# Performance work log

Measured on AMD Instinct MI355X. Metric: run time of the kernel, lower is better.

The kernel has to match this reference:

```python
import jax, jax.numpy as jnp
import numpy as np

UNITS = 256
D_IN = 256


def setup_inputs() -> dict:
    key = jax.random.key(0)
    ks = jax.random.split(key, 12)
    B, T, M, d, u = 16, 128, 512, D_IN, UNITS
    s = lambda fan_in: 1.0 / np.sqrt(fan_in)
    return {
        "inputs": jax.random.normal(ks[0], (B, T, d), jnp.float32),
        "attended_inputs": jax.random.normal(ks[1], (B, M, d), jnp.float32),
        # key_dense: Dense(units) applied to attended_inputs
        "key_W": jax.random.normal(ks[2], (d, u), jnp.float32) * s(d),
        "key_b": jnp.zeros((u,), jnp.float32),
        # query_dense: Dense(units) applied to state_h
        "query_W": jax.random.normal(ks[3], (u, u), jnp.float32) * s(u),
        "query_b": jnp.zeros((u,), jnp.float32),
        # attention_dense: Dense(1)
        "attn_W": jax.random.normal(ks[4], (u, 1), jnp.float32) * s(u),
        "attn_b": jnp.zeros((1,), jnp.float32),
        # LSTMCell built with input dim 2*d (inputs concat context); gate order i,f,g,o
        "lstm_W": jax.random.normal(ks[5], (2 * d, 4 * u), jnp.float32) * s(2 * d),
        "lstm_U": jax.random.normal(ks[6], (u, 4 * u), jnp.float32) * s(u),
        "lstm_b": jnp.zeros((4 * u,), jnp.float32),
    }


def reference(inputs, attended_inputs, key_W, key_b, query_W, query_b,
              attn_W, attn_b, lstm_W, lstm_U, lstm_b):
    B, T, d = inputs.shape
    u = lstm_U.shape[0]
    # keys computed once, shared across all timesteps: [B, M, u]
    keys = jnp.einsum('bmd,du->bmu', attended_inputs, key_W) + key_b
    aw = attn_W[:, 0]  # [u]

    def step(carry, x_t):
        h, c = carry                                   # [B,u], [B,u]
        q = h @ query_W + query_b                      # [B,u]
        e = jnp.tanh(keys + q[:, None, :])             # [B,M,u]
        scores = jnp.einsum('bmu,u->bm', e, aw) + attn_b[0]
        a = jax.nn.softmax(scores, axis=-1)            # [B,M]
        ctx = jnp.einsum('bm,bmd->bd', a, attended_inputs)
        xin = jnp.concatenate([x_t, ctx], axis=-1)     # [B,2d]
        z = xin @ lstm_W + h @ lstm_U + lstm_b         # [B,4u]
        i_g, f_g, g_g, o_g = jnp.split(z, 4, axis=-1)
        i_g = jax.nn.sigmoid(i_g)
        f_g = jax.nn.sigmoid(f_g)
        g_g = jnp.tanh(g_g)
        o_g = jax.nn.sigmoid(o_g)
        c_new = f_g * c + i_g * g_g
        h_new = o_g * jnp.tanh(c_new)
        return (h_new, c_new), h_new

    h0 = jnp.zeros((B, u), inputs.dtype)
    c0 = jnp.zeros((B, u), inputs.dtype)
    (hT, cT), ys = jax.lax.scan(step, (h0, c0), jnp.swapaxes(inputs, 0, 1))
    seq = jnp.swapaxes(ys, 0, 1)  # [B,T,u] (return_sequences=True)
    return seq, hT, cT
```

## Files before the change

kernel.cpp:

```cpp
#include <hip/hip_runtime.h>
#include <hip/hip_bf16.h>
#include <cstddef>

#define BATCH 16
#define TSTEPS 128
#define MSLOTS 512
#define DIN 256
#define UNITS 256
#define ZDIM 1024
#define G 8
#define NBLK (BATCH*G)
#define NTHR 1024

static __device__ __forceinline__ float tanhf_fast(float x) {
    float e = __expf(2.0f * x);
    return 1.0f - 2.0f / (e + 1.0f);
}
static __device__ __forceinline__ float sigmoidf_fast(float x) {
    return 1.0f / (1.0f + __expf(-x));
}
static __device__ __forceinline__ void st_agent_u(unsigned* p, unsigned v) {
    __hip_atomic_store(p, v, __ATOMIC_RELAXED, __HIP_MEMORY_SCOPE_AGENT);
}
static __device__ __forceinline__ unsigned ld_agent_u(const unsigned* p) {
    return __hip_atomic_load(p, __ATOMIC_RELAXED, __HIP_MEMORY_SCOPE_AGENT);
}
static __device__ __forceinline__ unsigned pack_bf(float a, float b) {
    unsigned ua = __float_as_uint(a); ua = (ua + 0x7fffu + ((ua >> 16) & 1u)) >> 16;
    unsigned ub = __float_as_uint(b); ub = ((ub + 0x7fffu + ((ub >> 16) & 1u)) >> 16) << 16;
    return ua | ub;
}
static __device__ __forceinline__ float bf_lo(unsigned w) { return __uint_as_float(w << 16); }
static __device__ __forceinline__ float bf_hi(unsigned w) { return __uint_as_float(w & 0xffff0000u); }

__global__ __launch_bounds__(256) void gemm_bias_kernel(
    const float* __restrict__ A, const float* __restrict__ B,
    const float* __restrict__ bias, float* __restrict__ C,
    int M, int N, int K)
{
    __shared__ float As[16][68];
    __shared__ float Bs[16][68];
    const int tid = threadIdx.x;
    const int bm = blockIdx.x * 64;
    const int bn = blockIdx.y * 64;
    const int tx = tid & 15, ty = tid >> 4;
    const int ar = tid >> 2, ac = (tid & 3) * 4;
    const int br = tid >> 4, bc = (tid & 15) * 4;
    float acc[4][4] = {};

    for (int k0 = 0; k0 < K; k0 += 16) {
        float4 av = *(const float4*)(A + (size_t)(bm + ar) * K + k0 + ac);
        float4 bv = *(const float4*)(B + (size_t)(k0 + br) * N + bn + bc);
        As[ac + 0][ar] = av.x; As[ac + 1][ar] = av.y;
        As[ac + 2][ar] = av.z; As[ac + 3][ar] = av.w;
        *(float4*)(&Bs[br][bc]) = bv;
        __syncthreads();
#pragma unroll
        for (int kk = 0; kk < 16; ++kk) {
            float a0 = As[kk][ty*4+0], a1 = As[kk][ty*4+1];
            float a2 = As[kk][ty*4+2], a3 = As[kk][ty*4+3];
            float b0 = Bs[kk][tx*4+0], b1 = Bs[kk][tx*4+1];
            float b2 = Bs[kk][tx*4+2], b3 = Bs[kk][tx*4+3];
            acc[0][0]+=a0*b0; acc[0][1]+=a0*b1; acc[0][2]+=a0*b2; acc[0][3]+=a0*b3;
            acc[1][0]+=a1*b0; acc[1][1]+=a1*b1; acc[1][2]+=a1*b2; acc[1][3]+=a1*b3;
            acc[2][0]+=a2*b0; acc[2][1]+=a2*b1; acc[2][2]+=a2*b2; acc[2][3]+=a2*b3;
            acc[3][0]+=a3*b0; acc[3][1]+=a3*b1; acc[3][2]+=a3*b2; acc[3][3]+=a3*b3;
        }
        __syncthreads();
    }
#pragma unroll
    for (int i = 0; i < 4; ++i)
#pragma unroll
        for (int j = 0; j < 4; ++j) {
            int cn = bn + tx * 4 + j;
            C[(size_t)(bm + ty * 4 + i) * N + cn] = acc[i][j] + bias[cn];
        }
}

__global__ __launch_bounds__(256) void gemm_T_bf16_kernel(
    const float* __restrict__ A, const float* __restrict__ B,
    unsigned short* __restrict__ CT, int M, int N, int K)
{
    __shared__ float As[16][68];
    __shared__ float Bs[16][68];
    __shared__ float Ts[64][65];
    const int tid = threadIdx.x;
    const int bm = blockIdx.x * 64;
    const int bn = blockIdx.y * 64;
    const int tx = tid & 15, ty = tid >> 4;
    const int ar = tid >> 2, ac = (tid & 3) * 4;
    const int br = tid >> 4, bc = (tid & 15) * 4;
    float acc[4][4] = {};

    for (int k0 = 0; k0 < K; k0 += 16) {
        float4 av = *(const float4*)(A + (size_t)(bm + ar) * K + k0 + ac);
        float4 bv = *(const float4*)(B + (size_t)(k0 + br) * N + bn + bc);
        As[ac + 0][ar] = av.x; As[ac + 1][ar] = av.y;
        As[ac + 2][ar] = av.z; As[ac + 3][ar] = av.w;
        *(float4*)(&Bs[br][bc]) = bv;
        __syncthreads();
#pragma unroll
        for (int kk = 0; kk < 16; ++kk) {
            float a0 = As[kk][ty*4+0], a1 = As[kk][ty*4+1];
            float a2 = As[kk][ty*4+2], a3 = As[kk][ty*4+3];
            float b0 = Bs[kk][tx*4+0], b1 = Bs[kk][tx*4+1];
            float b2 = Bs[kk][tx*4+2], b3 = Bs[kk][tx*4+3];
            acc[0][0]+=a0*b0; acc[0][1]+=a0*b1; acc[0][2]+=a0*b2; acc[0][3]+=a0*b3;
            acc[1][0]+=a1*b0; acc[1][1]+=a1*b1; acc[1][2]+=a1*b2; acc[1][3]+=a1*b3;
            acc[2][0]+=a2*b0; acc[2][1]+=a2*b1; acc[2][2]+=a2*b2; acc[2][3]+=a2*b3;
            acc[3][0]+=a3*b0; acc[3][1]+=a3*b1; acc[3][2]+=a3*b2; acc[3][3]+=a3*b3;
        }
        __syncthreads();
    }
#pragma unroll
    for (int i = 0; i < 4; ++i)
#pragma unroll
        for (int j = 0; j < 4; ++j)
            Ts[tx * 4 + j][ty * 4 + i] = acc[i][j];
    __syncthreads();
    const int jr = tid >> 2, ms2 = (tid & 3) * 16;
    const int b = bm >> 9, m0 = bm & 511;
    unsigned short* dst = CT + (size_t)b * ((size_t)N * 512)
                        + (size_t)(bn + jr) * 512 + m0 + ms2;
#pragma unroll
    for (int u = 0; u < 16; ++u) {
        unsigned ua = __float_as_uint(Ts[jr][ms2 + u]);
        ua = (ua + 0x7fffu + ((ua >> 16) & 1u)) >> 16;
        dst[u] = (unsigned short)ua;
    }
}

__global__ __launch_bounds__(NTHR, 4) void rnn_persistent(
    const float* __restrict__ query_W, const float* __restrict__ query_b,
    const float* __restrict__ attn_W,  const float* __restrict__ lstm_U,
    const float* __restrict__ keys,    const float* __restrict__ pre,
    const unsigned short* __restrict__ aw2T,
    unsigned* zcT, unsigned* zhp, unsigned* dP, unsigned* sent,
    float* __restrict__ seq, float* __restrict__ hT, float* __restrict__ cT)
{
    const int bid = blockIdx.x;
    const int b = bid >> 3, g = bid & 7;
    const int tid = threadIdx.x;

    __shared__ unsigned Wq2[128 * 256];
    __shared__ __align__(16) float h_s[256];
    __shared__ __align__(16) float c_s[256];
    __shared__ __align__(16) float q_s[256];
    __shared__ __align__(16) float qp_s[4][256];
    __shared__ __align__(16) float p_s[64];
    __shared__ __align__(16) float zp_s[8][128];
    __shared__ __align__(16) float z_s[1024];
    __shared__ __align__(16) float aw_s[256];
    __shared__ __align__(16) float qb_s[256];
    __shared__ float invd_s;

    const int jq = tid & 255, kq = tid >> 8;
    const int mloc = tid >> 4, jc = tid & 15;
    const int cc = tid & 127, ks = tid >> 7;
    const int col_own = ((cc >> 5) << 8) + g * 32 + (cc & 31);

    for (int i = tid; i < 128 * 256; i += NTHR) {
        int k2 = i >> 8, j = i & 255;
        Wq2[i] = pack_bf(query_W[(size_t)(2 * k2) * 256 + j],
                         query_W[(size_t)(2 * k2 + 1) * 256 + j]);
    }
    unsigned keys_r[8];
    {
        const float* krow = keys + (size_t)(b * MSLOTS + g * 64 + mloc) * 256;
#pragma unroll
        for (int i = 0; i < 8; ++i)
            keys_r[i] = pack_bf(krow[jc + 32 * i], krow[jc + 32 * i + 16]);
    }
    unsigned u_r[16];
#pragma unroll
    for (int i = 0; i < 16; ++i)
        u_r[i] = pack_bf(lstm_U[(size_t)(ks * 32 + 2 * i) * ZDIM + col_own],
                         lstm_U[(size_t)(ks * 32 + 2 * i + 1) * ZDIM + col_own]);
    unsigned aw2_r[32];
    {
        const unsigned* a0 = (const unsigned*)(aw2T + ((size_t)b * ZDIM + tid) * 512 + g * 64);
#pragma unroll
        for (int i = 0; i < 32; ++i) aw2_r[i] = a0[i];
    }

    if (tid < 256) {
        aw_s[tid] = attn_W[tid];
        qb_s[tid] = query_b[tid];
        h_s[tid] = 0.0f;
        c_s[tid] = 0.0f;
    }
    __syncthreads();

    const float* preb = pre + (size_t)b * TSTEPS * ZDIM;
    unsigned* sentb = sent + b * 16;

    for (int t = 0; t < TSTEPS; ++t) {
        const int par = t & 1;
        const unsigned tag = (unsigned)(t + 1);
        unsigned* zcb = zcT + (size_t)(par * BATCH + b) * 1024 * 8;
        unsigned* zhb = zhp + (size_t)(par * BATCH + b) * 1024;
        unsigned* dPb = dP + (size_t)(par * BATCH + b) * 8;

        float pre_r = 0.0f;
        if (tid < 128)
            pre_r = preb[(size_t)t * ZDIM + col_own];

        {
            float zh = 0.0f;
#pragma unroll
            for (int i = 0; i < 16; ++i) {
                float2 hv = *(const float2*)&h_s[ks * 32 + 2 * i];
                zh += hv.x * bf_lo(u_r[i]) + hv.y * bf_hi(u_r[i]);
            }
            zp_s[ks][cc] = zh;
        }
        {
            float qa = 0.0f;
#pragma unroll
            for (int i = 0; i < 32; ++i) {
                unsigned w = Wq2[(kq * 32 + i) * 256 + jq];
                float2 hv = *(const float2*)&h_s[kq * 64 + 2 * i];
                qa += hv.x * bf_lo(w) + hv.y * bf_hi(w);
            }
            qp_s[kq][jq] = qa;
        }
        __syncthreads();
        if (tid < 256)
            q_s[tid] = qb_s[tid] + qp_s[0][tid] + qp_s[1][tid] + qp_s[2][tid] + qp_s[3][tid];
        if (tid < 128) {
            float zv = pre_r + zp_s[0][tid] + zp_s[1][tid] + zp_s[2][tid] + zp_s[3][tid]
                     + zp_s[4][tid] + zp_s[5][tid] + zp_s[6][tid] + zp_s[7][tid];
            st_agent_u(&zhb[col_own], __float_as_uint(zv));
        }
        __syncthreads();

        {
            float sacc = 0.0f;
#pragma unroll
            for (int i = 0; i < 8; ++i) {
                int j0 = jc + 32 * i, j1 = j0 + 16;
                unsigned kw = keys_r[i];
                sacc += aw_s[j0] * tanhf_fast(bf_lo(kw) + q_s[j0]);
                sacc += aw_s[j1] * tanhf_fast(bf_hi(kw) + q_s[j1]);
            }
            sacc += __shfl_xor(sacc, 1);
            sacc += __shfl_xor(sacc, 2);
            sacc += __shfl_xor(sacc, 4);
            sacc += __shfl_xor(sacc, 8);
            if (jc == 0) p_s[mloc] = __expf(sacc);
        }
        __syncthreads();

        {
            float zcv = 0.0f;
#pragma unroll
            for (int i = 0; i < 32; ++i) {
                float2 pv = *(const float2*)&p_s[2 * i];
                zcv += pv.x * bf_lo(aw2_r[i]) + pv.y * bf_hi(aw2_r[i]);
            }
            st_agent_u(&zcb[(size_t)tid * 8 + g], __float_as_uint(zcv));
        }
        if (tid < 64) {
            float dv = p_s[tid];
            dv += __shfl_xor(dv, 1);  dv += __shfl_xor(dv, 2);  dv += __shfl_xor(dv, 4);
            dv += __shfl_xor(dv, 8);  dv += __shfl_xor(dv, 16); dv += __shfl_xor(dv, 32);
            if (tid == 0) st_agent_u(&dPb[g], __float_as_uint(dv));
        }

        __syncthreads();
        if (tid == 0) st_agent_u(&sentb[g], tag);
        if (tid < 8 && tid != g) {
            while (ld_agent_u(&sentb[tid]) < tag)
                __builtin_amdgcn_s_sleep(1);
        }
        __syncthreads();

        float zcsum;
        float zhv;
        {
            const unsigned* zrow = &zcb[(size_t)tid * 8];
            float s0 = __uint_as_float(ld_agent_u(&zrow[0]));
            float s1 = __uint_as_float(ld_agent_u(&zrow[1]));
            float s2 = __uint_as_float(ld_agent_u(&zrow[2]));
            float s3 = __uint_as_float(ld_agent_u(&zrow[3]));
            float s4 = __uint_as_float(ld_agent_u(&zrow[4]));
            float s5 = __uint_as_float(ld_agent_u(&zrow[5]));
            float s6 = __uint_as_float(ld_agent_u(&zrow[6]));
            float s7 = __uint_as_float(ld_agent_u(&zrow[7]));
            zcsum = ((s0 + s1) + (s2 + s3)) + ((s4 + s5) + (s6 + s7));
            zhv = __uint_as_float(ld_agent_u(&zhb[tid]));
        }
        if (tid < 8) {
            float dv = __uint_as_float(ld_agent_u(&dPb[tid]));
            dv += __shfl_xor(dv, 1); dv += __shfl_xor(dv, 2); dv += __shfl_xor(dv, 4);
            if (tid == 0) invd_s = 1.0f / dv;
        }
        __syncthreads();
        z_s[tid] = zhv + zcsum * invd_s;
        __syncthreads();

        if (tid < 256) {
            float zi = z_s[tid], zf = z_s[256 + tid], zg = z_s[512 + tid], zo = z_s[768 + tid];
            float ig = sigmoidf_fast(zi);
            float fg = sigmoidf_fast(zf);
            float gg = tanhf_fast(zg);
            float og = sigmoidf_fast(zo);
            float cn = fg * c_s[tid] + ig * gg;
            float hn = og * tanhf_fast(cn);
            c_s[tid] = cn;
            h_s[tid] = hn;
            if ((tid >> 5) == g) {
                seq[((size_t)b * TSTEPS + t) * UNITS + tid] = hn;
                if (t == TSTEPS - 1) { hT[b * UNITS + tid] = hn; cT[b * UNITS + tid] = cn; }
            }
        }
        __syncthreads();
    }
}

extern "C" void kernel_launch(void* const* d_in, const int* in_sizes, int n_in,
                              void* d_out, int out_size, void* d_ws, size_t ws_size,
                              hipStream_t stream)
{
    (void)in_sizes; (void)n_in; (void)out_size; (void)ws_size;
    const float* inputs   = (const float*)d_in[0];
    const float* attended = (const float*)d_in[1];
    const float* key_W    = (const float*)d_in[2];
    const float* key_b    = (const float*)d_in[3];
    const float* query_W  = (const float*)d_in[4];
    const float* query_b  = (const float*)d_in[5];
    const float* attn_W   = (const float*)d_in[6];
    const float* lstm_W   = (const float*)d_in[8];
    const float* lstm_U   = (const float*)d_in[9];
    const float* lstm_b   = (const float*)d_in[10];

    float* out = (float*)d_out;
    float* seq = out;
    float* hT  = out + (size_t)BATCH * TSTEPS * UNITS;
    float* cT  = hT + BATCH * UNITS;

    float* ws = (float*)d_ws;
    float* keys = ws;
    float* pre  = keys + 2097152;
    unsigned short* aw2T = (unsigned short*)(pre + 2097152);
    unsigned* zcT  = (unsigned*)(aw2T + (size_t)16 * 1024 * 512);
    unsigned* zhp  = zcT + 2 * BATCH * 1024 * 8;
    unsigned* dP   = zhp + 2 * BATCH * 1024;
    unsigned* sent = dP + 2 * BATCH * 8;

    hipMemsetAsync(sent, 0, (size_t)BATCH * 16 * sizeof(unsigned), stream);

    gemm_bias_kernel<<<dim3(128, 4), 256, 0, stream>>>(
        attended, key_W, key_b, keys, 8192, 256, 256);
    gemm_bias_kernel<<<dim3(32, 16), 256, 0, stream>>>(
        inputs, lstm_W, lstm_b, pre, 2048, 1024, 256);
    gemm_T_bf16_kernel<<<dim3(128, 16), 256, 0, stream>>>(
        attended, lstm_W + (size_t)256 * ZDIM, aw2T, 8192, 1024, 256);

    rnn_persistent<<<dim3(NBLK), dim3(NTHR), 0, stream>>>(
        query_W, query_b, attn_W, lstm_U,
        keys, pre, aw2T, zcT, zhp, dP, sent, seq, hT, cT);
}
```

Baseline: 1.778 ms.

## Repartition persistent RNN so each block owns 32 hidden units with two exchanges

The per-step work is split differently across the 8 blocks of a batch row. Before, every block computed partial context-gate sums for all 1024 gate columns and then exchanged them through global memory. Now blocks exchange only the 64 unnormalised attention probabilities each, compute context contributions for their own 128 gate columns from an LDS-resident slice of aw2T, and then exchange the 32 new hidden values. Query weights move from LDS into registers so the aw2T slice fits in LDS. This cuts the global traffic per step but adds a second inter-block barrier per step.

```diff
diff --git a/kernel.cpp b/kernel.cpp
--- a/kernel.cpp
+++ b/kernel.cpp
@@ -135,35 +135,40 @@
     const float* __restrict__ attn_W,  const float* __restrict__ lstm_U,
     const float* __restrict__ keys,    const float* __restrict__ pre,
     const unsigned short* __restrict__ aw2T,
-    unsigned* zcT, unsigned* zhp, unsigned* dP, unsigned* sent,
+    unsigned* pB, unsigned* hB, unsigned* sent,
     float* __restrict__ seq, float* __restrict__ hT, float* __restrict__ cT)
 {
     const int bid = blockIdx.x;
     const int b = bid >> 3, g = bid & 7;
     const int tid = threadIdx.x;
 
-    __shared__ unsigned Wq2[128 * 256];
+    __shared__ unsigned aw2L[256 * 128];
     __shared__ __align__(16) float h_s[256];
-    __shared__ __align__(16) float c_s[256];
     __shared__ __align__(16) float q_s[256];
     __shared__ __align__(16) float qp_s[4][256];
-    __shared__ __align__(16) float p_s[64];
+    __shared__ __align__(16) float p_s[512];
+    __shared__ __align__(16) float pown_s[64];
     __shared__ __align__(16) float zp_s[8][128];
-    __shared__ __align__(16) float z_s[1024];
+    __shared__ __align__(16) float z_s[128];
     __shared__ __align__(16) float aw_s[256];
     __shared__ __align__(16) float qb_s[256];
-    __shared__ float invd_s;
+    __shared__ __align__(16) float red_s[8];
 
     const int jq = tid & 255, kq = tid >> 8;
     const int mloc = tid >> 4, jc = tid & 15;
     const int cc = tid & 127, ks = tid >> 7;
     const int col_own = ((cc >> 5) << 8) + g * 32 + (cc & 31);
 
-    for (int i = tid; i < 128 * 256; i += NTHR) {
-        int k2 = i >> 8, j = i & 255;
-        Wq2[i] = pack_bf(query_W[(size_t)(2 * k2) * 256 + j],
-                         query_W[(size_t)(2 * k2 + 1) * 256 + j]);
-    }
+    for (int i = tid; i < 256 * 128; i += NTHR) {
+        int pr = i >> 7, c2 = i & 127;
+        int colc = ((c2 >> 5) << 8) + g * 32 + (c2 & 31);
+        aw2L[i] = ((const unsigned*)(aw2T + ((size_t)b * ZDIM + colc) * 512))[pr];
+    }
+    unsigned wq_r[32];
+#pragma unroll
+    for (int i = 0; i < 32; ++i)
+        wq_r[i] = pack_bf(query_W[(size_t)(kq * 64 + 2 * i) * 256 + jq],
+                          query_W[(size_t)(kq * 64 + 2 * i + 1) * 256 + jq]);
     unsigned keys_r[8];
     {
         const float* krow = keys + (size_t)(b * MSLOTS + g * 64 + mloc) * 256;
@@ -176,35 +181,37 @@
     for (int i = 0; i < 16; ++i)
         u_r[i] = pack_bf(lstm_U[(size_t)(ks * 32 + 2 * i) * ZDIM + col_own],
                          lstm_U[(size_t)(ks * 32 + 2 * i + 1) * ZDIM + col_own]);
-    unsigned aw2_r[32];
-    {
-        const unsigned* a0 = (const unsigned*)(aw2T + ((size_t)b * ZDIM + tid) * 512 + g * 64);
-#pragma unroll
-        for (int i = 0; i < 32; ++i) aw2_r[i] = a0[i];
-    }
 
     if (tid < 256) {
         aw_s[tid] = attn_W[tid];
         qb_s[tid] = query_b[tid];
         h_s[tid] = 0.0f;
-        c_s[tid] = 0.0f;
-    }
+    }
+    float c_r = 0.0f;
     __syncthreads();
 
     const float* preb = pre + (size_t)b * TSTEPS * ZDIM;
+    unsigned* pBb = pB + b * 512;
+    unsigned* hBb = hB + b * 256;
     unsigned* sentb = sent + b * 16;
 
     for (int t = 0; t < TSTEPS; ++t) {
-        const int par = t & 1;
-        const unsigned tag = (unsigned)(t + 1);
-        unsigned* zcb = zcT + (size_t)(par * BATCH + b) * 1024 * 8;
-        unsigned* zhb = zhp + (size_t)(par * BATCH + b) * 1024;
-        unsigned* dPb = dP + (size_t)(par * BATCH + b) * 8;
+        const unsigned ptag = (unsigned)(2 * t + 1);
+        const unsigned htag = (unsigned)(2 * t + 2);
 
         float pre_r = 0.0f;
         if (tid < 128)
             pre_r = preb[(size_t)t * ZDIM + col_own];
 
+        {
+            float qa = 0.0f;
+#pragma unroll
+            for (int i = 0; i < 32; ++i) {
+                float2 hv = *(const float2*)&h_s[kq * 64 + 2 * i];
+                qa += hv.x * bf_lo(wq_r[i]) + hv.y * bf_hi(wq_r[i]);
+            }
+            qp_s[kq][jq] = qa;
+        }
         {
             float zh = 0.0f;
 #pragma unroll
@@ -214,24 +221,14 @@
             }
             zp_s[ks][cc] = zh;
         }
-        {
-            float qa = 0.0f;
-#pragma unroll
-            for (int i = 0; i < 32; ++i) {
-                unsigned w = Wq2[(kq * 32 + i) * 256 + jq];
-                float2 hv = *(const float2*)&h_s[kq * 64 + 2 * i];
-                qa += hv.x * bf_lo(w) + hv.y * bf_hi(w);
-            }
-            qp_s[kq][jq] = qa;
-        }
-        __syncthreads();
+        __syncthreads();
+
         if (tid < 256)
             q_s[tid] = qb_s[tid] + qp_s[0][tid] + qp_s[1][tid] + qp_s[2][tid] + qp_s[3][tid];
-        if (tid < 128) {
-            float zv = pre_r + zp_s[0][tid] + zp_s[1][tid] + zp_s[2][tid] + zp_s[3][tid]
-                     + zp_s[4][tid] + zp_s[5][tid] + zp_s[6][tid] + zp_s[7][tid];
-            st_agent_u(&zhb[col_own], __float_as_uint(zv));
-        }
+        float zv = 0.0f;
+        if (tid < 128)
+            zv = pre_r + zp_s[0][cc] + zp_s[1][cc] + zp_s[2][cc] + zp_s[3][cc]
+               + zp_s[4][cc] + zp_s[5][cc] + zp_s[6][cc] + zp_s[7][cc];
         __syncthreads();
 
         {
@@ -247,73 +244,82 @@
             sacc += __shfl_xor(sacc, 2);
             sacc += __shfl_xor(sacc, 4);
             sacc += __shfl_xor(sacc, 8);
-            if (jc == 0) p_s[mloc] = __expf(sacc);
-        }
-        __syncthreads();
-
-        {
-            float zcv = 0.0f;
-#pragma unroll
-            for (int i = 0; i < 32; ++i) {
-                float2 pv = *(const float2*)&p_s[2 * i];
-                zcv += pv.x * bf_lo(aw2_r[i]) + pv.y * bf_hi(aw2_r[i]);
-            }
-            st_agent_u(&zcb[(size_t)tid * 8 + g], __float_as_uint(zcv));
-        }
+            if (jc == 0) pown_s[mloc] = __expf(sacc);
+        }
+        __syncthreads();
+
         if (tid < 64) {
-            float dv = p_s[tid];
+            st_agent_u(&pBb[g * 64 + tid], __float_as_uint(pown_s[tid]));
+            asm volatile("s_waitcnt vmcnt(0)" ::: "memory");
+            if (tid == 0) st_agent_u(&sentb[g], ptag);
+        }
+        if (tid < 8 && tid != g) {
+            while (ld_agent_u(&sentb[tid]) < ptag)
+                __builtin_amdgcn_s_sleep(1);
+        }
+        __syncthreads();
+        if (tid < 512) {
+            float pv;
+            if ((tid >> 6) == g) pv = pown_s[tid & 63];
+            else                 pv = __uint_as_float(ld_agent_u(&pBb[tid]));
+            p_s[tid] = pv;
+            float dv = pv;
             dv += __shfl_xor(dv, 1);  dv += __shfl_xor(dv, 2);  dv += __shfl_xor(dv, 4);
             dv += __shfl_xor(dv, 8);  dv += __shfl_xor(dv, 16); dv += __shfl_xor(dv, 32);
-            if (tid == 0) st_agent_u(&dPb[g], __float_as_uint(dv));
-        }
-
-        __syncthreads();
-        if (tid == 0) st_agent_u(&sentb[g], tag);
-        if (tid < 8 && tid != g) {
-            while (ld_agent_u(&sentb[tid]) < tag)
-                __builtin_amdgcn_s_sleep(1);
-        }
-        __syncthreads();
-
-        float zcsum;
-        float zhv;
-        {
-            const unsigned* zrow = &zcb[(size_t)tid * 8];
-            float s0 = __uint_as_float(ld_agent_u(&zrow[0]));
-            float s1 = __uint_as_float(ld_agent_u(&zrow[1]));
-            float s2 = __uint_as_float(ld_agent_u(&zrow[2]));
-            float s3 = __uint_as_float(ld_agent_u(&zrow[3]));
-            float s4 = __uint_as_float(ld_agent_u(&zrow[4]));
-            float s5 = __uint_as_float(ld_agent_u(&zrow[5]));
-            float s6 = __uint_as_float(ld_agent_u(&zrow[6]));
-            float s7 = __uint_as_float(ld_agent_u(&zrow[7]));
-            zcsum = ((s0 + s1) + (s2 + s3)) + ((s4 + s5) + (s6 + s7));
-            zhv = __uint_as_float(ld_agent_u(&zhb[tid]));
-        }
-        if (tid < 8) {
-            float dv = __uint_as_float(ld_agent_u(&dPb[tid]));
-            dv += __shfl_xor(dv, 1); dv += __shfl_xor(dv, 2); dv += __shfl_xor(dv, 4);
-            if (tid == 0) invd_s = 1.0f / dv;
-        }
-        __syncthreads();
-        z_s[tid] = zhv + zcsum * invd_s;
-        __syncthreads();
-
-        if (tid < 256) {
-            float zi = z_s[tid], zf = z_s[256 + tid], zg = z_s[512 + tid], zo = z_s[768 + tid];
+            if ((tid & 63) == 0) red_s[tid >> 6] = dv;
+        }
+        __syncthreads();
+        float inv;
+        {
+            float tot = red_s[0] + red_s[1] + red_s[2] + red_s[3]
+                      + red_s[4] + red_s[5] + red_s[6] + red_s[7];
+            inv = 1.0f / tot;
+        }
+
+        {
+            float zc = 0.0f;
+#pragma unroll
+            for (int i = 0; i < 32; ++i) {
+                float2 pv = *(const float2*)&p_s[ks * 64 + 2 * i];
+                unsigned w = aw2L[(ks * 32 + i) * 128 + cc];
+                zc += pv.x * bf_lo(w) + pv.y * bf_hi(w);
+            }
+            zp_s[ks][cc] = zc;
+        }
+        __syncthreads();
+        if (tid < 128) {
+            float zcs = zp_s[0][cc] + zp_s[1][cc] + zp_s[2][cc] + zp_s[3][cc]
+                      + zp_s[4][cc] + zp_s[5][cc] + zp_s[6][cc] + zp_s[7][cc];
+            z_s[cc] = zv + zcs * inv;
+        }
+        __syncthreads();
+
+        if (tid < 32) {
+            float zi = z_s[tid], zf = z_s[32 + tid], zg = z_s[64 + tid], zo = z_s[96 + tid];
             float ig = sigmoidf_fast(zi);
             float fg = sigmoidf_fast(zf);
             float gg = tanhf_fast(zg);
             float og = sigmoidf_fast(zo);
-            float cn = fg * c_s[tid] + ig * gg;
+            float cn = fg * c_r + ig * gg;
             float hn = og * tanhf_fast(cn);
-            c_s[tid] = cn;
-            h_s[tid] = hn;
-            if ((tid >> 5) == g) {
-                seq[((size_t)b * TSTEPS + t) * UNITS + tid] = hn;
-                if (t == TSTEPS - 1) { hT[b * UNITS + tid] = hn; cT[b * UNITS + tid] = cn; }
-            }
-        }
+            c_r = cn;
+            int u = g * 32 + tid;
+            h_s[u] = hn;
+            st_agent_u(&hBb[u], __float_as_uint(hn));
+            seq[((size_t)b * TSTEPS + t) * UNITS + u] = hn;
+            if (t == TSTEPS - 1) { hT[b * UNITS + u] = hn; cT[b * UNITS + u] = cn; }
+        }
+        if (tid < 64) {
+            asm volatile("s_waitcnt vmcnt(0)" ::: "memory");
+            if (tid == 0) st_agent_u(&sentb[8 + g], htag);
+        }
+        if (tid < 8 && tid != g) {
+            while (ld_agent_u(&sentb[8 + tid]) < htag)
+                __builtin_amdgcn_s_sleep(1);
+        }
+        __syncthreads();
+        if (tid < 256 && (tid >> 5) != g)
+            h_s[tid] = __uint_as_float(ld_agent_u(&hBb[tid]));
         __syncthreads();
     }
 }
@@ -343,10 +349,9 @@
     float* keys = ws;
     float* pre  = keys + 2097152;
     unsigned short* aw2T = (unsigned short*)(pre + 2097152);
-    unsigned* zcT  = (unsigned*)(aw2T + (size_t)16 * 1024 * 512);
-    unsigned* zhp  = zcT + 2 * BATCH * 1024 * 8;
-    unsigned* dP   = zhp + 2 * BATCH * 1024;
-    unsigned* sent = dP + 2 * BATCH * 8;
+    unsigned* pB   = (unsigned*)(aw2T + (size_t)16 * 1024 * 512);
+    unsigned* hB   = pB + BATCH * 512;
+    unsigned* sent = hB + BATCH * 256;
 
     hipMemsetAsync(sent, 0, (size_t)BATCH * 16 * sizeof(unsigned), stream);
 
@@ -359,5 +364,5 @@
 
     rnn_persistent<<<dim3(NBLK), dim3(NTHR), 0, stream>>>(
         query_W, query_b, attn_W, lstm_U,
-        keys, pre, aw2T, zcT, zhp, dP, sent, seq, hT, cT);
-}
+        keys, pre, aw2T, pB, hB, sent, seq, hT, cT);
+}
```

Measured after the change: 1.607 ms. -9.6%, faster.
